# Kernel optimization log

Hardware: AMD Instinct MI355X
Metric: run time of the kernel (lower is better)

The kernel has to match this reference:

```python
import jax, jax.numpy as jnp
import numpy as np

X_DIM = 362
N_EXPERTS = 3
HIDDEN = [1024, 2048, 2048, 1024]  # layer widths; final layer maps back to X_DIM


def _init_params(key):
    dims = [X_DIM] + HIDDEN + [X_DIM]
    params = {}
    for li in range(len(dims) - 1):
        fan_in = dims[li]
        kW, kb, key = jax.random.split(key, 3)
        bound = 1.0 / np.sqrt(fan_in)
        # stacked over experts: [E, in, out]
        params[f"W{li}"] = jax.random.uniform(kW, (N_EXPERTS, dims[li], dims[li + 1]), jnp.float32, -bound, bound)
        params[f"b{li}"] = jax.random.uniform(kb, (N_EXPERTS, dims[li + 1]), jnp.float32, -bound, bound)
    return params


def setup_inputs() -> dict:
    key = jax.random.key(0)
    kx, kn, ka, kp = jax.random.split(key, 4)
    B = 8192
    inp = {
        "batch_x": jax.random.normal(kx, (B, X_DIM), jnp.float32),
        "batch_next": jax.random.normal(kn, (B, X_DIM), jnp.float32),
        "batch_a": jax.random.randint(ka, (B,), 0, N_EXPERTS, jnp.int64),
    }
    inp.update(_init_params(kp))
    return inp


def _experts_forward(x, W0, b0, W1, b1, W2, b2, W3, b3, W4, b4):
    # Run every expert on the full batch (dense grouped GEMMs), then select.
    # h: [E, B, d]
    h = jax.nn.relu(jnp.einsum("bi,eio->ebo", x, W0) + b0[:, None, :])
    h = jax.nn.relu(jnp.einsum("ebi,eio->ebo", h, W1) + b1[:, None, :])
    h = jax.nn.relu(jnp.einsum("ebi,eio->ebo", h, W2) + b2[:, None, :])
    h = jax.nn.relu(jnp.einsum("ebi,eio->ebo", h, W3) + b3[:, None, :])
    return jnp.einsum("ebi,eio->ebo", h, W4) + b4[:, None, :]  # [E, B, X_DIM]


def reference(batch_x, batch_next, batch_a, W0, b0, W1, b1, W2, b2, W3, b3, W4, b4):
    preds = _experts_forward(batch_x, W0, b0, W1, b1, W2, b2, W3, b3, W4, b4)
    # route: pick each sample's prediction from its action's expert
    pred_next = preds[batch_a, jnp.arange(batch_x.shape[0])]  # [B, X_DIM]
    return jnp.mean((pred_next - batch_next) ** 2)
```

## Files before the change

kernel.cpp:

```cpp
#include <hip/hip_runtime.h>
#include <hip/hip_bf16.h>

#define B_SZ   8192
#define XD     362
#define NEXP   3
#define NTILES 70
#define MP     (NTILES*128)

typedef __bf16 bf16x8 __attribute__((ext_vector_type(8)));
typedef float  f32x4  __attribute__((ext_vector_type(4)));

__device__ __forceinline__ unsigned short f2bf(float f) {
    unsigned u = __float_as_uint(f);
    u += 0x7fffu + ((u >> 16) & 1u);
    return (unsigned short)(u >> 16);
}

__global__ __launch_bounds__(1024) void k_route(const int* __restrict__ a,
                                                int* __restrict__ hdr,
                                                int* __restrict__ row_of) {
    __shared__ int sc[3][1024];
    int tid = threadIdx.x;
    int ev[8];
    int c0 = 0, c1 = 0, c2 = 0;
#pragma unroll
    for (int j = 0; j < 8; ++j) {
        int e = a[tid * 8 + j];
        ev[j] = e;
        c0 += (e == 0); c1 += (e == 1); c2 += (e == 2);
    }
    sc[0][tid] = c0; sc[1][tid] = c1; sc[2][tid] = c2;
    __syncthreads();
    for (int off = 1; off < 1024; off <<= 1) {
        int v0 = (tid >= off) ? sc[0][tid - off] : 0;
        int v1 = (tid >= off) ? sc[1][tid - off] : 0;
        int v2 = (tid >= off) ? sc[2][tid - off] : 0;
        __syncthreads();
        sc[0][tid] += v0; sc[1][tid] += v1; sc[2][tid] += v2;
        __syncthreads();
    }
    int tot0 = sc[0][1023], tot1 = sc[1][1023], tot2 = sc[2][1023];
    int t0 = ((tot0 + 255) >> 8) << 1;
    int t1 = ((tot1 + 255) >> 8) << 1;
    int t2 = ((tot2 + 255) >> 8) << 1;
    int seg0 = 0, seg1 = t0 * 128, seg2 = (t0 + t1) * 128;
    int nt = t0 + t1 + t2;
    int b0 = seg0 + sc[0][tid] - c0;
    int b1 = seg1 + sc[1][tid] - c1;
    int b2 = seg2 + sc[2][tid] - c2;
#pragma unroll
    for (int j = 0; j < 8; ++j) {
        int e = ev[j];
        int pos = (e == 0) ? b0++ : (e == 1) ? b1++ : b2++;
        row_of[pos] = tid * 8 + j;
    }
    if (tid == 0) {
        hdr[0] = tot0; hdr[1] = tot1; hdr[2] = tot2;
        hdr[6] = seg0; hdr[7] = seg1; hdr[8] = seg2;
        hdr[12] = nt;
        hdr[16] = 0;
    }
    if (tid < NTILES)
        hdr[32 + tid] = (tid < t0) ? 0 : (tid < t0 + t1) ? 1 : (tid < nt) ? 2 : -1;
    for (int r = tid; r < MP; r += 1024) {
        int pad;
        if (r < seg1)           pad = (r - seg0) >= tot0;
        else if (r < seg2)      pad = (r - seg1) >= tot1;
        else if (r < nt * 128)  pad = (r - seg2) >= tot2;
        else                    pad = 1;
        if (pad) row_of[r] = -1;
    }
}

__global__ void k_gather(const float* __restrict__ x, const int* __restrict__ row_of,
                         unsigned short* __restrict__ xg) {
    int r = blockIdx.x;
    int c = threadIdx.x;
    int orig = row_of[r];
    float v = (orig >= 0 && c < XD) ? x[(size_t)orig * XD + c] : 0.f;
    xg[(size_t)r * 384 + c] = f2bf(v);
}

__global__ void k_transpose(const float* __restrict__ W, unsigned short* __restrict__ Wt,
                            int K, int N, int Kp, int Np) {
    __shared__ float t[64][33];
    int e  = blockIdx.z;
    int kb = blockIdx.x * 64, nb = blockIdx.y * 32;
    const float* We = W + (size_t)e * K * N;
    unsigned short* Wte = Wt + (size_t)e * Np * Kp;
    int tx = threadIdx.x, ty = threadIdx.y;
#pragma unroll
    for (int j = 0; j < 8; ++j) {
        int k = kb + ty + j * 8, n = nb + tx;
        t[ty + j * 8][tx] = (k < K && n < N) ? We[(size_t)k * N + n] : 0.f;
    }
    __syncthreads();
#pragma unroll
    for (int j = 0; j < 4; ++j) {
        int n = ty + j * 8;
        unsigned int lo = f2bf(t[2 * tx][n]);
        unsigned int hi = f2bf(t[2 * tx + 1][n]);
        *(unsigned int*)&Wte[(size_t)(nb + n) * Kp + kb + 2 * tx] = lo | (hi << 16);
    }
}

template <int TM, int TN, int WAVES, bool FINAL>
__global__ __launch_bounds__(WAVES * 64) void k_gemm(
    const unsigned short* __restrict__ A, int lda,
    const unsigned short* __restrict__ Bt, int K, int Np,
    const float* __restrict__ bias, int nvalid,
    unsigned short* __restrict__ C, int ldc,
    const int* __restrict__ hdr,
    const float* __restrict__ nextv, const int* __restrict__ row_of,
    float* __restrict__ accum)
{
    __shared__ unsigned short As[2][TM * 64];
    __shared__ unsigned short Bs[2][TN * 64];
    __shared__ float red[WAVES];

    constexpr int WGN = TN / 64;
    constexpr int LA  = TM / (WAVES * 8);
    constexpr int LB  = TN / (WAVES * 8);

    int mt = blockIdx.y;
    int e  = hdr[32 + mt * (TM / 128)];
    if (e < 0) return;
    int row0 = mt * TM;
    int n0   = blockIdx.x * TN;

    int tid  = threadIdx.x;
    int wid  = tid >> 6, lane = tid & 63;
    int quad = lane >> 4, l15 = lane & 15;
    int sw   = l15 & 7;
    int wm = (wid / WGN) * 64, wn = (wid % WGN) * 64;

    const unsigned short* Ag = A  + (size_t)row0 * lda;
    const unsigned short* Bg = Bt + (size_t)e * Np * K + (size_t)n0 * K;
    const float* be = bias + (size_t)e * nvalid;

    int srow = lane >> 3;
    int scol = ((lane & 7) ^ srow) * 8;

    f32x4 acc[4][4];
#pragma unroll
    for (int i = 0; i < 4; ++i)
#pragma unroll
        for (int j = 0; j < 4; ++j)
            acc[i][j] = (f32x4){0.f, 0.f, 0.f, 0.f};

#define STAGE(K0, P)                                                              \
    {                                                                             \
        _Pragma("unroll")                                                         \
        for (int ii = 0; ii < LA; ++ii) {                                         \
            int rbase = wid * (TM / WAVES) + ii * 8;                              \
            const unsigned short* gp = Ag + (size_t)(rbase + srow) * lda + (K0) + scol; \
            __builtin_amdgcn_global_load_lds(                                     \
                (const __attribute__((address_space(1))) void*)gp,                \
                (__attribute__((address_space(3))) void*)(As[P] + rbase * 64), 16, 0, 0); \
        }                                                                         \
        _Pragma("unroll")                                                         \
        for (int ii = 0; ii < LB; ++ii) {                                         \
            int rbase = wid * (TN / WAVES) + ii * 8;                              \
            const unsigned short* gp = Bg + (size_t)(rbase + srow) * K + (K0) + scol;   \
            __builtin_amdgcn_global_load_lds(                                     \
                (const __attribute__((address_space(1))) void*)gp,                \
                (__attribute__((address_space(3))) void*)(Bs[P] + rbase * 64), 16, 0, 0); \
        }                                                                         \
    }

#define COMPUTE(P)                                                                \
    {                                                                             \
        _Pragma("unroll")                                                         \
        for (int kh = 0; kh < 2; ++kh) {                                          \
            bf16x8 af[4], bfr[4];                                                 \
            _Pragma("unroll")                                                     \
            for (int f = 0; f < 4; ++f) {                                         \
                int row = wm + f * 16 + l15;                                      \
                af[f] = *(const bf16x8*)(As[P] + row * 64 + (((kh * 4 + quad) ^ sw) << 3)); \
            }                                                                     \
            _Pragma("unroll")                                                     \
            for (int f = 0; f < 4; ++f) {                                         \
                int row = wn + f * 16 + l15;                                      \
                bfr[f] = *(const bf16x8*)(Bs[P] + row * 64 + (((kh * 4 + quad) ^ sw) << 3)); \
            }                                                                     \
            _Pragma("unroll")                                                     \
            for (int fm = 0; fm < 4; ++fm)                                        \
                _Pragma("unroll")                                                 \
                for (int fn = 0; fn < 4; ++fn)                                    \
                    acc[fm][fn] = __builtin_amdgcn_mfma_f32_16x16x32_bf16(        \
                        af[fm], bfr[fn], acc[fm][fn], 0, 0, 0);                   \
        }                                                                         \
    }

    STAGE(0, 0);
    __syncthreads();
    for (int k0 = 0; k0 < K; k0 += 128) {
        if (k0 + 64 < K) STAGE(k0 + 64, 1);
        COMPUTE(0);
        __syncthreads();
        if (k0 + 128 < K) STAGE(k0 + 128, 0);
        COMPUTE(1);
        __syncthreads();
    }
#undef STAGE
#undef COMPUTE

    if constexpr (!FINAL) {
#pragma unroll
        for (int fn = 0; fn < 4; ++fn) {
            int n = n0 + wn + fn * 16 + l15;
            float bv = be[n];
#pragma unroll
            for (int fm = 0; fm < 4; ++fm) {
#pragma unroll
                for (int i = 0; i < 4; ++i) {
                    int r = row0 + wm + fm * 16 + quad * 4 + i;
                    float v = acc[fm][fn][i] + bv;
                    v = v > 0.f ? v : 0.f;
                    C[(size_t)r * ldc + n] = f2bf(v);
                }
            }
        }
    } else {
        float local = 0.f;
#pragma unroll
        for (int fm = 0; fm < 4; ++fm) {
#pragma unroll
            for (int i = 0; i < 4; ++i) {
                int r = row0 + wm + fm * 16 + quad * 4 + i;
                int orig = row_of[r];
                if (orig >= 0) {
                    const float* nrow = nextv + (size_t)orig * XD;
#pragma unroll
                    for (int fn = 0; fn < 4; ++fn) {
                        int n = n0 + wn + fn * 16 + l15;
                        if (n < XD) {
                            float v = acc[fm][fn][i] + be[n];
                            float d = v - nrow[n];
                            local += d * d;
                        }
                    }
                }
            }
        }
        for (int off = 32; off > 0; off >>= 1)
            local += __shfl_down(local, off, 64);
        if (lane == 0) red[wid] = local;
        __syncthreads();
        if (tid == 0) {
            float s = 0.f;
#pragma unroll
            for (int w = 0; w < WAVES; ++w) s += red[w];
            atomicAdd(accum, s);
        }
    }
}

__global__ void k_final(const int* hdr, float* out) {
    if (blockIdx.x == 0 && threadIdx.x == 0) {
        float s = ((const float*)hdr)[16];
        out[0] = s / (float)(B_SZ * XD);
    }
}

extern "C" void kernel_launch(void* const* d_in, const int* in_sizes, int n_in,
                              void* d_out, int out_size, void* d_ws, size_t ws_size,
                              hipStream_t stream) {
    const float* x     = (const float*)d_in[0];
    const float* nextv = (const float*)d_in[1];
    const int*   a     = (const int*)d_in[2];
    const float* W0 = (const float*)d_in[3],  *b0 = (const float*)d_in[4];
    const float* W1 = (const float*)d_in[5],  *b1 = (const float*)d_in[6];
    const float* W2 = (const float*)d_in[7],  *b2 = (const float*)d_in[8];
    const float* W3 = (const float*)d_in[9],  *b3 = (const float*)d_in[10];
    const float* W4 = (const float*)d_in[11], *b4 = (const float*)d_in[12];

    int* hdr    = (int*)d_ws;
    int* row_of = hdr + 128;
    unsigned short* xg = (unsigned short*)(row_of + MP);
    unsigned short* hA = xg + (size_t)MP * 384;
    unsigned short* hB = hA + (size_t)MP * 2048;
    unsigned short* Wt = hB + (size_t)MP * 2048;
    float* accum = (float*)(hdr + 16);

    k_route <<<1, 1024, 0, stream>>>(a, hdr, row_of);
    k_gather<<<MP, 384, 0, stream>>>(x, row_of, xg);

    k_transpose<<<dim3(6, 32, 3), dim3(32, 8), 0, stream>>>(W0, Wt, XD, 1024, 384, 1024);
    k_gemm<128, 128, 4, false><<<dim3(8, NTILES), 256, 0, stream>>>(
        xg, 384, Wt, 384, 1024, b0, 1024, hA, 1024, hdr, nullptr, nullptr, nullptr);
    k_transpose<<<dim3(16, 64, 3), dim3(32, 8), 0, stream>>>(W1, Wt, 1024, 2048, 1024, 2048);
    k_gemm<256, 256, 16, false><<<dim3(8, NTILES / 2), 1024, 0, stream>>>(
        hA, 1024, Wt, 1024, 2048, b1, 2048, hB, 2048, hdr, nullptr, nullptr, nullptr);
    k_transpose<<<dim3(32, 64, 3), dim3(32, 8), 0, stream>>>(W2, Wt, 2048, 2048, 2048, 2048);
    k_gemm<256, 256, 16, false><<<dim3(8, NTILES / 2), 1024, 0, stream>>>(
        hB, 2048, Wt, 2048, 2048, b2, 2048, hA, 2048, hdr, nullptr, nullptr, nullptr);
    k_transpose<<<dim3(32, 32, 3), dim3(32, 8), 0, stream>>>(W3, Wt, 2048, 1024, 2048, 1024);
    k_gemm<256, 128, 8, false><<<dim3(8, NTILES / 2), 512, 0, stream>>>(
        hA, 2048, Wt, 2048, 1024, b3, 1024, hB, 1024, hdr, nullptr, nullptr, nullptr);
    k_transpose<<<dim3(16, 12, 3), dim3(32, 8), 0, stream>>>(W4, Wt, 1024, XD, 1024, 384);
    k_gemm<128, 128, 4, true><<<dim3(3, NTILES), 256, 0, stream>>>(
        hB, 1024, Wt, 1024, 384, b4, XD, nullptr, 0, hdr, nextv, row_of, accum);

    k_final<<<1, 64, 0, stream>>>(hdr, (float*)d_out);
}
```

Before: 537.9 us.

## Add 32x32x16 MFMA GEMM with direct global-to-LDS loads for hidden layers

Adds a new GEMM kernel for the three large hidden layers. It uses 32x32x16 bf16 MFMA, 256-row by 256-column tiles with 4 waves each owning a 128x128 sub-tile, and global_load_lds to stream A and B straight into swizzled, double-buffered LDS. The aim is fewer LDS reads per FLOP, no register round-trip on loads, and higher MFMA throughput than the 16x16-based kernel run with 16 waves. In exchange it carries a large accumulator register footprint at one block per CU, and the epilogue writes C with scattered scalar 16-bit stores.

```diff
diff --git a/kernel.cpp b/kernel.cpp
--- a/kernel.cpp
+++ b/kernel.cpp
@@ -9,6 +9,7 @@
 
 typedef __bf16 bf16x8 __attribute__((ext_vector_type(8)));
 typedef float  f32x4  __attribute__((ext_vector_type(4)));
+typedef float  f32x16 __attribute__((ext_vector_type(16)));
 
 __device__ __forceinline__ unsigned short f2bf(float f) {
     unsigned u = __float_as_uint(f);
@@ -105,7 +106,7 @@
 }
 
 template <int TM, int TN, int WAVES, bool FINAL>
-__global__ __launch_bounds__(WAVES * 64) void k_gemm(
+__global__ __launch_bounds__(WAVES * 64) void k_gemm16(
     const unsigned short* __restrict__ A, int lda,
     const unsigned short* __restrict__ Bt, int K, int Np,
     const float* __restrict__ bias, int nvalid,
@@ -256,6 +257,115 @@
     }
 }
 
+__global__ __launch_bounds__(256, 1) void k_gemm32(
+    const unsigned short* __restrict__ A, int lda,
+    const unsigned short* __restrict__ Bt, int K, int Np,
+    const float* __restrict__ bias, int nvalid,
+    unsigned short* __restrict__ C, int ldc,
+    const int* __restrict__ hdr)
+{
+    __shared__ unsigned short As[2][256 * 64];
+    __shared__ unsigned short Bs[2][256 * 64];
+
+    int mt = blockIdx.y;
+    int e  = hdr[32 + mt * 2];
+    if (e < 0) return;
+    int row0 = mt * 256;
+    int n0   = blockIdx.x * 256;
+
+    int tid  = threadIdx.x;
+    int wid  = tid >> 6, lane = tid & 63;
+    int l31  = lane & 31, khi = lane >> 5;
+    int sw   = l31 & 7;
+    int wm = (wid >> 1) * 128, wn = (wid & 1) * 128;
+
+    const unsigned short* Ag = A  + (size_t)row0 * lda;
+    const unsigned short* Bg = Bt + (size_t)e * Np * K + (size_t)n0 * K;
+    const float* be = bias + (size_t)e * nvalid;
+
+    int srow = lane >> 3;
+    int scol = ((lane & 7) ^ srow) * 8;
+
+    f32x16 acc[4][4];
+#pragma unroll
+    for (int i = 0; i < 4; ++i)
+#pragma unroll
+        for (int j = 0; j < 4; ++j)
+#pragma unroll
+            for (int v = 0; v < 16; ++v)
+                acc[i][j][v] = 0.f;
+
+#define STAGE(K0, P)                                                              \
+    {                                                                             \
+        _Pragma("unroll")                                                         \
+        for (int ii = 0; ii < 8; ++ii) {                                          \
+            int rbase = wid * 64 + ii * 8;                                        \
+            const unsigned short* gpA = Ag + (size_t)(rbase + srow) * lda + (K0) + scol; \
+            __builtin_amdgcn_global_load_lds(                                     \
+                (const __attribute__((address_space(1))) void*)gpA,               \
+                (__attribute__((address_space(3))) void*)(As[P] + rbase * 64), 16, 0, 0); \
+            const unsigned short* gpB = Bg + (size_t)(rbase + srow) * K + (K0) + scol;   \
+            __builtin_amdgcn_global_load_lds(                                     \
+                (const __attribute__((address_space(1))) void*)gpB,               \
+                (__attribute__((address_space(3))) void*)(Bs[P] + rbase * 64), 16, 0, 0); \
+        }                                                                         \
+    }
+
+#define COMPUTE(P)                                                                \
+    {                                                                             \
+        _Pragma("unroll")                                                         \
+        for (int ks = 0; ks < 4; ++ks) {                                          \
+            int cb = ks * 2 + khi;                                                \
+            bf16x8 af[4], bfr[4];                                                 \
+            _Pragma("unroll")                                                     \
+            for (int f = 0; f < 4; ++f) {                                         \
+                int row = wm + f * 32 + l31;                                      \
+                af[f] = *(const bf16x8*)(As[P] + row * 64 + ((cb ^ sw) << 3));    \
+            }                                                                     \
+            _Pragma("unroll")                                                     \
+            for (int f = 0; f < 4; ++f) {                                         \
+                int row = wn + f * 32 + l31;                                      \
+                bfr[f] = *(const bf16x8*)(Bs[P] + row * 64 + ((cb ^ sw) << 3));   \
+            }                                                                     \
+            _Pragma("unroll")                                                     \
+            for (int fm = 0; fm < 4; ++fm)                                        \
+                _Pragma("unroll")                                                 \
+                for (int fn = 0; fn < 4; ++fn)                                    \
+                    acc[fm][fn] = __builtin_amdgcn_mfma_f32_32x32x16_bf16(        \
+                        af[fm], bfr[fn], acc[fm][fn], 0, 0, 0);                   \
+        }                                                                         \
+    }
+
+    STAGE(0, 0);
+    __syncthreads();
+    for (int k0 = 0; k0 < K; k0 += 128) {
+        if (k0 + 64 < K) STAGE(k0 + 64, 1);
+        COMPUTE(0);
+        __syncthreads();
+        if (k0 + 128 < K) STAGE(k0 + 128, 0);
+        COMPUTE(1);
+        __syncthreads();
+    }
+#undef STAGE
+#undef COMPUTE
+
+#pragma unroll
+    for (int fn = 0; fn < 4; ++fn) {
+        int n = n0 + wn + fn * 32 + l31;
+        float bv = be[n];
+#pragma unroll
+        for (int fm = 0; fm < 4; ++fm) {
+#pragma unroll
+            for (int i = 0; i < 16; ++i) {
+                int r = row0 + wm + fm * 32 + (i & 3) + 8 * (i >> 2) + 4 * khi;
+                float v = acc[fm][fn][i] + bv;
+                v = v > 0.f ? v : 0.f;
+                C[(size_t)r * ldc + n] = f2bf(v);
+            }
+        }
+    }
+}
+
 __global__ void k_final(const int* hdr, float* out) {
     if (blockIdx.x == 0 && threadIdx.x == 0) {
         float s = ((const float*)hdr)[16];
@@ -287,19 +397,19 @@
     k_gather<<<MP, 384, 0, stream>>>(x, row_of, xg);
 
     k_transpose<<<dim3(6, 32, 3), dim3(32, 8), 0, stream>>>(W0, Wt, XD, 1024, 384, 1024);
-    k_gemm<128, 128, 4, false><<<dim3(8, NTILES), 256, 0, stream>>>(
+    k_gemm16<128, 128, 4, false><<<dim3(8, NTILES), 256, 0, stream>>>(
         xg, 384, Wt, 384, 1024, b0, 1024, hA, 1024, hdr, nullptr, nullptr, nullptr);
     k_transpose<<<dim3(16, 64, 3), dim3(32, 8), 0, stream>>>(W1, Wt, 1024, 2048, 1024, 2048);
-    k_gemm<256, 256, 16, false><<<dim3(8, NTILES / 2), 1024, 0, stream>>>(
-        hA, 1024, Wt, 1024, 2048, b1, 2048, hB, 2048, hdr, nullptr, nullptr, nullptr);
+    k_gemm32<<<dim3(8, NTILES / 2), 256, 0, stream>>>(
+        hA, 1024, Wt, 1024, 2048, b1, 2048, hB, 2048, hdr);
     k_transpose<<<dim3(32, 64, 3), dim3(32, 8), 0, stream>>>(W2, Wt, 2048, 2048, 2048, 2048);
-    k_gemm<256, 256, 16, false><<<dim3(8, NTILES / 2), 1024, 0, stream>>>(
-        hB, 2048, Wt, 2048, 2048, b2, 2048, hA, 2048, hdr, nullptr, nullptr, nullptr);
+    k_gemm32<<<dim3(8, NTILES / 2), 256, 0, stream>>>(
+        hB, 2048, Wt, 2048, 2048, b2, 2048, hA, 2048, hdr);
     k_transpose<<<dim3(32, 32, 3), dim3(32, 8), 0, stream>>>(W3, Wt, 2048, 1024, 2048, 1024);
-    k_gemm<256, 128, 8, false><<<dim3(8, NTILES / 2), 512, 0, stream>>>(
-        hA, 2048, Wt, 2048, 1024, b3, 1024, hB, 1024, hdr, nullptr, nullptr, nullptr);
+    k_gemm32<<<dim3(4, NTILES / 2), 256, 0, stream>>>(
+        hA, 2048, Wt, 2048, 1024, b3, 1024, hB, 1024, hdr);
     k_transpose<<<dim3(16, 12, 3), dim3(32, 8), 0, stream>>>(W4, Wt, 1024, XD, 1024, 384);
-    k_gemm<128, 128, 4, true><<<dim3(3, NTILES), 256, 0, stream>>>(
+    k_gemm16<128, 128, 4, true><<<dim3(3, NTILES), 256, 0, stream>>>(
         hB, 1024, Wt, 1024, 384, b4, XD, nullptr, 0, hdr, nextv, row_of, accum);
 
     k_final<<<1, 64, 0, stream>>>(hdr, (float*)d_out);
```

Result: slower. 599.7 us (+11.5%).
